# Kernel optimization log

Hardware: AMD Instinct MI355X
Metric: run time of the kernel (lower is better)

The kernel has to match this reference:

```python
import jax, jax.numpy as jnp
import numpy as np

C = 512        # feat_dim
T_LEN = 8192   # sequence length
N = 16384      # number of proposals
HID = 1024     # hidden_dim
OUT = 512      # out_dim
RATIO = 0.15   # boundary_ratio


def setup_inputs() -> dict:
    key = jax.random.key(0)
    ks = jax.random.split(key, 6)
    feat_map = jax.random.normal(ks[0], (C, T_LEN), jnp.float32)
    l = jax.random.randint(ks[1], (N,), 0, T_LEN - 64)
    width = jax.random.randint(ks[2], (N,), 8, 512)
    r = jnp.minimum(l + width, T_LEN - 1)
    W1 = jax.random.normal(ks[3], (HID, 2 * C), jnp.float32) * 0.02
    b1 = jnp.zeros((HID,), jnp.float32)
    W2 = jax.random.normal(ks[4], (OUT, HID), jnp.float32) * 0.02
    b2 = jnp.zeros((OUT,), jnp.float32)
    return {
        "feat_map": feat_map,
        "l": l.astype(jnp.int32),
        "r": r.astype(jnp.int32),
        "T": T_LEN,
        "W1": W1, "b1": b1, "W2": W2, "b2": b2,
    }


def _boundary_regions(l, r, T):
    # Mirrors: w = max(r-l, 1.0); bw = max(1, int(ratio*w)); clipped windows.
    lf = l.astype(jnp.float32)
    rf = r.astype(jnp.float32)
    w = jnp.maximum(rf - lf, 1.0)
    bw = jnp.maximum(1, (RATIO * w).astype(jnp.int32))  # int() truncation (w > 0)
    rl = jnp.round(lf).astype(jnp.int32)
    rr = jnp.round(rf).astype(jnp.int32)
    lb_s = jnp.maximum(0, rl - bw)
    lb_e = jnp.minimum(T, rl + bw)
    rb_s = jnp.maximum(0, rr - bw)
    rb_e = jnp.minimum(T, rr + bw)
    return lb_s, lb_e, rb_s, rb_e


def _pool(cs, s, e, T):
    # mean of feat[:, s:e] via inclusive prefix sums; cs: (C, T+1)
    e = jnp.maximum(s + 1, e)
    e = jnp.minimum(e, T)
    seg = cs[:, e] - cs[:, s]                      # (C, N)
    return (seg / (e - s).astype(cs.dtype)).T      # (N, C)


def reference(feat_map, l, r, T, W1, b1, W2, b2):
    # feat_map: (C, T); l, r: (N,) int proposal boundaries
    cs = jnp.concatenate(
        [jnp.zeros((feat_map.shape[0], 1), feat_map.dtype),
         jnp.cumsum(feat_map, axis=1)], axis=1)    # (C, T+1)
    lb_s, lb_e, rb_s, rb_e = _boundary_regions(l, r, T)
    e_left = _pool(cs, lb_s, lb_e, T)              # (N, C)
    e_right = _pool(cs, rb_s, rb_e, T)             # (N, C)
    e = jnp.concatenate([e_left, e_right], axis=-1)  # (N, 2C)
    h = jax.nn.relu(e @ W1.T + b1)                 # (N, HID)
    return h @ W2.T + b2                           # (N, OUT)
```

## Files before the change

kernel.cpp:

```cpp
#include <hip/hip_runtime.h>
#include <hip/hip_bf16.h>
#include <stdint.h>

#define C_DIM 512
#define T_SEQ 8192
#define N_PROP 16384
#define HID_DIM 1024
#define OUT_DIM 512
#define K2C 1024

typedef __attribute__((ext_vector_type(8))) __bf16 bf16x8;
typedef __attribute__((ext_vector_type(4))) float f32x4;

__global__ __launch_bounds__(256) void cumsum_kernel(const float* __restrict__ feat,
                                                     float* __restrict__ cs_inc) {
    int c = blockIdx.x;
    const float4* in = (const float4*)(feat + (size_t)c * T_SEQ);
    float4* out = (float4*)(cs_inc + (size_t)c * T_SEQ);
    const int lane = threadIdx.x & 63;
    const int w = threadIdx.x >> 6;
    __shared__ float wsum[4];

    float4 v[8];
    float carry = 0.0f;
#pragma unroll
    for (int i = 0; i < 8; ++i) {
        float4 t = in[w * 512 + i * 64 + lane];
        float a1 = t.x + t.y;
        float a2 = a1 + t.z;
        float a3 = a2 + t.w;
        float x = a3;
#pragma unroll
        for (int s = 1; s < 64; s <<= 1) {
            float y = __shfl_up(x, s);
            if (lane >= s) x += y;
        }
        float base = carry + (x - a3);
        v[i].x = base + t.x;
        v[i].y = base + a1;
        v[i].z = base + a2;
        v[i].w = base + a3;
        carry += __shfl(x, 63);
    }
    if (lane == 0) wsum[w] = carry;
    __syncthreads();
    float pre = 0.0f;
    for (int j = 0; j < 4; ++j)
        if (j < w) pre += wsum[j];
#pragma unroll
    for (int i = 0; i < 8; ++i) {
        float4 o;
        o.x = v[i].x + pre; o.y = v[i].y + pre; o.z = v[i].z + pre; o.w = v[i].w + pre;
        out[w * 512 + i * 64 + lane] = o;
    }
}

__global__ __launch_bounds__(256) void transpose_kernel(const float* __restrict__ cs_inc,
                                                        float* __restrict__ cs_t) {
    __shared__ float tl[32][33];
    int tx = threadIdx.x, ty = threadIdx.y;
    int x0 = blockIdx.x * 32;
    int y0 = blockIdx.y * 32;
#pragma unroll
    for (int i = 0; i < 32; i += 8) {
        int t = x0 + tx;
        int ch = y0 + ty + i;
        float v = 0.0f;
        if (t >= 1 && t <= T_SEQ) v = cs_inc[(size_t)ch * T_SEQ + (t - 1)];
        tl[ty + i][tx] = v;
    }
    __syncthreads();
#pragma unroll
    for (int i = 0; i < 32; i += 8) {
        int t = x0 + ty + i;
        int ch = y0 + tx;
        if (t <= T_SEQ) cs_t[(size_t)t * C_DIM + ch] = tl[tx][ty + i];
    }
}

__global__ __launch_bounds__(512) void pool_kernel(const float* __restrict__ cs_t,
                                                   const int* __restrict__ lptr,
                                                   const int* __restrict__ rptr,
                                                   __hip_bfloat16* __restrict__ e) {
    int n = blockIdx.x * 4 + (threadIdx.x >> 7);
    int c4 = (threadIdx.x & 127) * 4;
    int li = lptr[n], ri = rptr[n];
    float w = fmaxf((float)(ri - li), 1.0f);
    int bw = max(1, (int)(0.15f * w));
    int lb_s = max(0, li - bw);
    int lb_e = min(T_SEQ, li + bw);
    int rb_s = max(0, ri - bw);
    int rb_e = min(T_SEQ, ri + bw);
    lb_e = min(max(lb_s + 1, lb_e), T_SEQ);
    rb_e = min(max(rb_s + 1, rb_e), T_SEQ);
    float4 a = *(const float4*)(cs_t + (size_t)lb_e * C_DIM + c4);
    float4 b = *(const float4*)(cs_t + (size_t)lb_s * C_DIM + c4);
    float4 cc = *(const float4*)(cs_t + (size_t)rb_e * C_DIM + c4);
    float4 d = *(const float4*)(cs_t + (size_t)rb_s * C_DIM + c4);
    float rl = 1.0f / (float)(lb_e - lb_s);
    float rr = 1.0f / (float)(rb_e - rb_s);
    __hip_bfloat16 L0 = __float2bfloat16((a.x - b.x) * rl);
    __hip_bfloat16 L1 = __float2bfloat16((a.y - b.y) * rl);
    __hip_bfloat16 L2 = __float2bfloat16((a.z - b.z) * rl);
    __hip_bfloat16 L3 = __float2bfloat16((a.w - b.w) * rl);
    __hip_bfloat16 R0 = __float2bfloat16((cc.x - d.x) * rr);
    __hip_bfloat16 R1 = __float2bfloat16((cc.y - d.y) * rr);
    __hip_bfloat16 R2 = __float2bfloat16((cc.z - d.z) * rr);
    __hip_bfloat16 R3 = __float2bfloat16((cc.w - d.w) * rr);
    ushort4 ul, ur;
    ul.x = *(unsigned short*)&L0; ul.y = *(unsigned short*)&L1;
    ul.z = *(unsigned short*)&L2; ul.w = *(unsigned short*)&L3;
    ur.x = *(unsigned short*)&R0; ur.y = *(unsigned short*)&R1;
    ur.z = *(unsigned short*)&R2; ur.w = *(unsigned short*)&R3;
    *(ushort4*)(e + (size_t)n * K2C + c4) = ul;
    *(ushort4*)(e + (size_t)n * K2C + C_DIM + c4) = ur;
}

__global__ __launch_bounds__(256) void cvt_bf16_kernel(const float* __restrict__ W1,
                                                       const float* __restrict__ W2,
                                                       __hip_bfloat16* __restrict__ W1b,
                                                       __hip_bfloat16* __restrict__ W2b) {
    const int n1 = HID_DIM * K2C;
    int i = (blockIdx.x * 256 + threadIdx.x) * 4;
    const float* src;
    __hip_bfloat16* dst;
    int j;
    if (i < n1) { src = W1; dst = W1b; j = i; }
    else        { src = W2; dst = W2b; j = i - n1; }
    float4 v = *(const float4*)(src + j);
    __hip_bfloat16 h0 = __float2bfloat16(v.x);
    __hip_bfloat16 h1 = __float2bfloat16(v.y);
    __hip_bfloat16 h2 = __float2bfloat16(v.z);
    __hip_bfloat16 h3 = __float2bfloat16(v.w);
    ushort4 u;
    u.x = *(unsigned short*)&h0; u.y = *(unsigned short*)&h1;
    u.z = *(unsigned short*)&h2; u.w = *(unsigned short*)&h3;
    *(ushort4*)(dst + j) = u;
}

template <int BM, int BN, int WM, int WN, int K, int RELU_BF16>
__global__ __launch_bounds__(512, 2) void gemm_hi_kernel(const __hip_bfloat16* __restrict__ A,
                                                         const __hip_bfloat16* __restrict__ B,
                                                         const float* __restrict__ bias,
                                                         void* __restrict__ Cout,
                                                         int Nc, int NBlk) {
    constexpr int BK = 32;
    constexpr int NT = K / BK;
    constexpr int WMT = BM / WM, WNT = BN / WN;
    constexpr int MR = WMT / 16, NR = WNT / 16;
    constexpr int RA = BM / 128;
    constexpr int RB = BN / 128;
    constexpr bool BHALF = (BN % 128) == 64;

    __shared__ __align__(16) __hip_bfloat16 As[2][BM * BK];
    __shared__ __align__(16) __hip_bfloat16 Bs[2][BN * BK];

    const int tid = threadIdx.x;
    const int lane = tid & 63;
    const int wid = tid >> 6;
    const int wm = wid / WN;
    const int wn = wid % WN;

    const int nwg = gridDim.x;
    const int wg = (blockIdx.x & 7) * (nwg >> 3) + (blockIdx.x >> 3);
    const long m0 = (long)(wg / NBlk) * BM;
    const long n0 = (long)(wg % NBlk) * BN;

    const int phase = ((blockIdx.x >> 8) & 1) * (NT / 2);

    const int srow = tid >> 2;
    const int sgsw = (tid & 3) ^ (srow & 3);
    const int fr = lane & 15;
    const int gq = lane >> 4;

    f32x4 acc[MR][NR] = {};

    auto stage = [&](int s, int k0) {
#pragma unroll
        for (int i = 0; i < RA; ++i)
            __builtin_amdgcn_global_load_lds(
                (const __attribute__((address_space(1))) void*)(A + (m0 + i * 128 + srow) * K + k0 + sgsw * 8),
                (__attribute__((address_space(3))) void*)(&As[s][i * 4096 + tid * 8]), 16, 0, 0);
#pragma unroll
        for (int i = 0; i < RB; ++i)
            __builtin_amdgcn_global_load_lds(
                (const __attribute__((address_space(1))) void*)(B + (n0 + i * 128 + srow) * K + k0 + sgsw * 8),
                (__attribute__((address_space(3))) void*)(&Bs[s][i * 4096 + tid * 8]), 16, 0, 0);
        if constexpr (BHALF) {
            if (tid < 256)
                __builtin_amdgcn_global_load_lds(
                    (const __attribute__((address_space(1))) void*)(B + (n0 + srow) * K + k0 + sgsw * 8),
                    (__attribute__((address_space(3))) void*)(&Bs[s][tid * 8]), 16, 0, 0);
        }
    };
    auto ldA = [&](int s, int row) -> bf16x8 {
        return *(const bf16x8*)(&As[s][row * BK + ((gq ^ (row & 3)) * 8)]);
    };
    auto ldB = [&](int s, int row) -> bf16x8 {
        return *(const bf16x8*)(&Bs[s][row * BK + ((gq ^ (row & 3)) * 8)]);
    };

    stage(0, phase * BK);
    __syncthreads();
    for (int t = 0; t < NT; ++t) {
        const int cur = t & 1;
        if (t + 1 < NT) stage(cur ^ 1, (((t + 1 + phase) & (NT - 1)) * BK));
        bf16x8 af[MR], bv[NR];
#pragma unroll
        for (int m = 0; m < MR; ++m) af[m] = ldA(cur, wm * WMT + m * 16 + fr);
#pragma unroll
        for (int n = 0; n < NR; ++n) bv[n] = ldB(cur, wn * WNT + n * 16 + fr);
#pragma unroll
        for (int m = 0; m < MR; ++m)
#pragma unroll
            for (int n = 0; n < NR; ++n)
                acc[m][n] = __builtin_amdgcn_mfma_f32_16x16x32_bf16(af[m], bv[n], acc[m][n], 0, 0, 0);
        __syncthreads();
    }

    const int rq = (lane >> 4) * 4;
#pragma unroll
    for (int m = 0; m < MR; ++m)
#pragma unroll
        for (int n = 0; n < NR; ++n) {
            long col = n0 + wn * WNT + n * 16 + fr;
            float bb = bias[col];
#pragma unroll
            for (int q = 0; q < 4; ++q) {
                long row = m0 + wm * WMT + m * 16 + rq + q;
                float v = acc[m][n][q] + bb;
                if (RELU_BF16) {
                    v = fmaxf(v, 0.0f);
                    ((__hip_bfloat16*)Cout)[row * Nc + col] = __float2bfloat16(v);
                } else {
                    ((float*)Cout)[row * Nc + col] = v;
                }
            }
        }
}

extern "C" void kernel_launch(void* const* d_in, const int* in_sizes, int n_in,
                              void* d_out, int out_size, void* d_ws, size_t ws_size,
                              hipStream_t stream) {
    const float* feat = (const float*)d_in[0];
    const int* l = (const int*)d_in[1];
    const int* r = (const int*)d_in[2];
    const float* W1 = (const float*)d_in[4];
    const float* b1 = (const float*)d_in[5];
    const float* W2 = (const float*)d_in[6];
    const float* b2 = (const float*)d_in[7];

    char* ws = (char*)d_ws;
    float* cs_t = (float*)ws;
    __hip_bfloat16* e = (__hip_bfloat16*)(ws + 16779264);
    __hip_bfloat16* h = (__hip_bfloat16*)(ws + 50333696);
    float* cs_inc = (float*)(ws + 50333696);
    __hip_bfloat16* W1b = (__hip_bfloat16*)(ws + 83888128);
    __hip_bfloat16* W2b = (__hip_bfloat16*)(ws + 85985280);

    const int ncvt = (HID_DIM * K2C + OUT_DIM * HID_DIM) / 4 / 256;
    cvt_bf16_kernel<<<dim3(ncvt), 256, 0, stream>>>(W1, W2, W1b, W2b);
    cumsum_kernel<<<dim3(C_DIM), 256, 0, stream>>>(feat, cs_inc);
    transpose_kernel<<<dim3((T_SEQ + 32) / 32, C_DIM / 32), dim3(32, 8), 0, stream>>>(cs_inc, cs_t);
    pool_kernel<<<dim3(N_PROP / 4), 512, 0, stream>>>(cs_t, l, r, e);

    gemm_hi_kernel<256, 128, 4, 2, K2C, 1>
        <<<dim3((N_PROP / 256) * (HID_DIM / 128)), 512, 0, stream>>>(e, W1b, b1, h, HID_DIM, HID_DIM / 128);
    gemm_hi_kernel<256, 64, 8, 1, HID_DIM, 0>
        <<<dim3((N_PROP / 256) * (OUT_DIM / 64)), 512, 0, stream>>>(h, W2b, b2, d_out, OUT_DIM, OUT_DIM / 64);
}
```

Before: 117.7 us.

## Rewrite GEMM kernels with BK=64, larger tiles and fine-grained staged pipeline

Replaces the simple double-buffered GEMM with a hand-scheduled kernel that uses BK=64, a 256x256 or 256x128 tile per workgroup, and interleaves half-tile async global-to-LDS loads with MFMA groups separated by explicit barriers, waitcnts and setprio. The goal is to overlap memory staging with matrix-core work and raise arithmetic intensity per LDS load. In exchange, occupancy drops to one workgroup per CU, the grid gets smaller, and the many barriers add synchronization overhead.

```diff
diff --git a/kernel.cpp b/kernel.cpp
--- a/kernel.cpp
+++ b/kernel.cpp
@@ -11,6 +11,9 @@
 
 typedef __attribute__((ext_vector_type(8))) __bf16 bf16x8;
 typedef __attribute__((ext_vector_type(4))) float f32x4;
+
+#define BAR() __builtin_amdgcn_s_barrier()
+#define LGKM0_SB() do { asm volatile("s_waitcnt lgkmcnt(0)" ::: "memory"); __builtin_amdgcn_sched_barrier(0); } while (0)
 
 __global__ __launch_bounds__(256) void cumsum_kernel(const float* __restrict__ feat,
                                                      float* __restrict__ cs_inc) {
@@ -138,19 +141,18 @@
     *(ushort4*)(dst + j) = u;
 }
 
-template <int BM, int BN, int WM, int WN, int K, int RELU_BF16>
-__global__ __launch_bounds__(512, 2) void gemm_hi_kernel(const __hip_bfloat16* __restrict__ A,
+template <int BN, int K, int RELU_BF16>
+__global__ __launch_bounds__(512, 1) void gemm_hk_kernel(const __hip_bfloat16* __restrict__ A,
                                                          const __hip_bfloat16* __restrict__ B,
                                                          const float* __restrict__ bias,
                                                          void* __restrict__ Cout,
                                                          int Nc, int NBlk) {
-    constexpr int BK = 32;
-    constexpr int NT = K / BK;
-    constexpr int WMT = BM / WM, WNT = BN / WN;
-    constexpr int MR = WMT / 16, NR = WNT / 16;
-    constexpr int RA = BM / 128;
-    constexpr int RB = BN / 128;
-    constexpr bool BHALF = (BN % 128) == 64;
+    constexpr int BM = 256, BK = 64;
+    constexpr int NT = K / BK, NI = NT / 2;
+    constexpr int WNT = BN / 4;
+    constexpr int NR = WNT / 16;
+    constexpr int RBH = BN / 128;
+    constexpr int BHR = BN / 2;
 
     __shared__ __align__(16) __hip_bfloat16 As[2][BM * BK];
     __shared__ __align__(16) __hip_bfloat16 Bs[2][BN * BK];
@@ -158,76 +160,126 @@
     const int tid = threadIdx.x;
     const int lane = tid & 63;
     const int wid = tid >> 6;
-    const int wm = wid / WN;
-    const int wn = wid % WN;
+    const int wm = wid >> 2;
+    const int wn = wid & 3;
 
     const int nwg = gridDim.x;
     const int wg = (blockIdx.x & 7) * (nwg >> 3) + (blockIdx.x >> 3);
     const long m0 = (long)(wg / NBlk) * BM;
     const long n0 = (long)(wg % NBlk) * BN;
 
-    const int phase = ((blockIdx.x >> 8) & 1) * (NT / 2);
-
-    const int srow = tid >> 2;
-    const int sgsw = (tid & 3) ^ (srow & 3);
+    const int srow = tid >> 3;
+    const int schunk = (tid & 7) ^ (srow & 7);
     const int fr = lane & 15;
-    const int gq = lane >> 4;
-
-    f32x4 acc[MR][NR] = {};
-
-    auto stage = [&](int s, int k0) {
-#pragma unroll
-        for (int i = 0; i < RA; ++i)
+    const int g8 = (lane >> 4) * 8;
+
+    f32x4 acc[8][NR] = {};
+
+    auto stA = [&](int d, int h, long kel) {
+#pragma unroll
+        for (int r2 = 0; r2 < 2; ++r2)
             __builtin_amdgcn_global_load_lds(
-                (const __attribute__((address_space(1))) void*)(A + (m0 + i * 128 + srow) * K + k0 + sgsw * 8),
-                (__attribute__((address_space(3))) void*)(&As[s][i * 4096 + tid * 8]), 16, 0, 0);
-#pragma unroll
-        for (int i = 0; i < RB; ++i)
+                (const __attribute__((address_space(1))) void*)(A + (m0 + h * 128 + r2 * 64 + srow) * K + kel + schunk * 8),
+                (__attribute__((address_space(3))) void*)(&As[d][(h * 128 + r2 * 64) * 64 + tid * 8]), 16, 0, 0);
+    };
+    auto stB = [&](int d, int h, long kel) {
+#pragma unroll
+        for (int r2 = 0; r2 < RBH; ++r2)
             __builtin_amdgcn_global_load_lds(
-                (const __attribute__((address_space(1))) void*)(B + (n0 + i * 128 + srow) * K + k0 + sgsw * 8),
-                (__attribute__((address_space(3))) void*)(&Bs[s][i * 4096 + tid * 8]), 16, 0, 0);
-        if constexpr (BHALF) {
-            if (tid < 256)
-                __builtin_amdgcn_global_load_lds(
-                    (const __attribute__((address_space(1))) void*)(B + (n0 + srow) * K + k0 + sgsw * 8),
-                    (__attribute__((address_space(3))) void*)(&Bs[s][tid * 8]), 16, 0, 0);
-        }
-    };
-    auto ldA = [&](int s, int row) -> bf16x8 {
-        return *(const bf16x8*)(&As[s][row * BK + ((gq ^ (row & 3)) * 8)]);
-    };
-    auto ldB = [&](int s, int row) -> bf16x8 {
-        return *(const bf16x8*)(&Bs[s][row * BK + ((gq ^ (row & 3)) * 8)]);
-    };
-
-    stage(0, phase * BK);
-    __syncthreads();
-    for (int t = 0; t < NT; ++t) {
-        const int cur = t & 1;
-        if (t + 1 < NT) stage(cur ^ 1, (((t + 1 + phase) & (NT - 1)) * BK));
-        bf16x8 af[MR], bv[NR];
-#pragma unroll
-        for (int m = 0; m < MR; ++m) af[m] = ldA(cur, wm * WMT + m * 16 + fr);
-#pragma unroll
-        for (int n = 0; n < NR; ++n) bv[n] = ldB(cur, wn * WNT + n * 16 + fr);
-#pragma unroll
-        for (int m = 0; m < MR; ++m)
+                (const __attribute__((address_space(1))) void*)(B + (n0 + h * BHR + r2 * 64 + srow) * K + kel + schunk * 8),
+                (__attribute__((address_space(3))) void*)(&Bs[d][(h * BHR + r2 * 64) * 64 + tid * 8]), 16, 0, 0);
+    };
+    auto ldf = [&](const __hip_bfloat16* buf, int row, int kb) -> bf16x8 {
+        return *(const bf16x8*)(&buf[row * 64 + ((kb + g8) ^ ((row & 7) * 8))]);
+    };
+    auto rdA = [&](int d, int mlo, int kb, bf16x8* af) {
+#pragma unroll
+        for (int m = 0; m < 4; ++m) af[m] = ldf(&As[d][0], wm * 128 + (mlo + m) * 16 + fr, kb);
+    };
+    auto rdB = [&](int d, int kb, bf16x8* bv) {
+#pragma unroll
+        for (int n = 0; n < NR; ++n) bv[n] = ldf(&Bs[d][0], wn * WNT + n * 16 + fr, kb);
+    };
+    auto mf4 = [&](const bf16x8* af, const bf16x8* bv, int mlo) {
+        __builtin_amdgcn_s_setprio(1);
+#pragma unroll
+        for (int m = 0; m < 4; ++m)
 #pragma unroll
             for (int n = 0; n < NR; ++n)
-                acc[m][n] = __builtin_amdgcn_mfma_f32_16x16x32_bf16(af[m], bv[n], acc[m][n], 0, 0, 0);
-        __syncthreads();
+                acc[mlo + m][n] = __builtin_amdgcn_mfma_f32_16x16x32_bf16(af[m], bv[n], acc[mlo + m][n], 0, 0, 0);
+        __builtin_amdgcn_s_setprio(0);
+    };
+
+    stA(0, 0, 0); stA(0, 1, 0); stB(0, 0, 0); stB(0, 1, 0);
+    stB(1, 0, BK);
+    asm volatile("s_waitcnt vmcnt(%0)" ::"n"(RBH) : "memory");
+    BAR();
+
+    bf16x8 afA[4], afB[4], bv[NR];
+
+#pragma unroll 1
+    for (int i = 0; i < NI; ++i) {
+        const bool more = (i + 1 < NI);
+        const long kU1 = (2L * i + 1) * BK;
+        const long kE = (2L * i + 2) * BK;
+        const long kO = (2L * i + 3) * BK;
+
+        rdA(0, 0, 0, afA); rdB(0, 0, bv);
+        stB(1, 1, kU1);
+        BAR(); LGKM0_SB();
+        mf4(afA, bv, 0);
+        BAR();
+        rdA(0, 4, 0, afB);
+        stA(1, 0, kU1);
+        BAR(); LGKM0_SB();
+        mf4(afB, bv, 4);
+        BAR();
+        rdA(0, 0, 32, afA); rdB(0, 32, bv);
+        stA(1, 1, kU1);
+        BAR(); LGKM0_SB();
+        mf4(afA, bv, 0);
+        BAR();
+        rdA(0, 4, 32, afB);
+        if (more) stB(0, 0, kE);
+        BAR(); LGKM0_SB();
+        mf4(afB, bv, 4);
+        if (more) asm volatile("s_waitcnt vmcnt(%0)" ::"n"(RBH) : "memory");
+        else      asm volatile("s_waitcnt vmcnt(0)" ::: "memory");
+        BAR();
+        rdA(1, 0, 0, afA); rdB(1, 0, bv);
+        if (more) stB(0, 1, kE);
+        BAR(); LGKM0_SB();
+        mf4(afA, bv, 0);
+        BAR();
+        rdA(1, 4, 0, afB);
+        if (more) stA(0, 0, kE);
+        BAR(); LGKM0_SB();
+        mf4(afB, bv, 4);
+        BAR();
+        rdA(1, 0, 32, afA); rdB(1, 32, bv);
+        if (more) stA(0, 1, kE);
+        BAR(); LGKM0_SB();
+        mf4(afA, bv, 0);
+        BAR();
+        rdA(1, 4, 32, afB);
+        if (more) stB(1, 0, kO);
+        BAR(); LGKM0_SB();
+        mf4(afB, bv, 4);
+        if (more) asm volatile("s_waitcnt vmcnt(%0)" ::"n"(RBH) : "memory");
+        else      asm volatile("s_waitcnt vmcnt(0)" ::: "memory");
+        BAR();
     }
 
     const int rq = (lane >> 4) * 4;
 #pragma unroll
-    for (int m = 0; m < MR; ++m)
+    for (int m = 0; m < 8; ++m)
 #pragma unroll
         for (int n = 0; n < NR; ++n) {
             long col = n0 + wn * WNT + n * 16 + fr;
             float bb = bias[col];
 #pragma unroll
             for (int q = 0; q < 4; ++q) {
-                long row = m0 + wm * WMT + m * 16 + rq + q;
+                long row = m0 + wm * 128 + m * 16 + rq + q;
                 float v = acc[m][n][q] + bb;
                 if (RELU_BF16) {
                     v = fmaxf(v, 0.0f);
@@ -264,8 +316,8 @@
     transpose_kernel<<<dim3((T_SEQ + 32) / 32, C_DIM / 32), dim3(32, 8), 0, stream>>>(cs_inc, cs_t);
     pool_kernel<<<dim3(N_PROP / 4), 512, 0, stream>>>(cs_t, l, r, e);
 
-    gemm_hi_kernel<256, 128, 4, 2, K2C, 1>
-        <<<dim3((N_PROP / 256) * (HID_DIM / 128)), 512, 0, stream>>>(e, W1b, b1, h, HID_DIM, HID_DIM / 128);
-    gemm_hi_kernel<256, 64, 8, 1, HID_DIM, 0>
-        <<<dim3((N_PROP / 256) * (OUT_DIM / 64)), 512, 0, stream>>>(h, W2b, b2, d_out, OUT_DIM, OUT_DIM / 64);
-}
+    gemm_hk_kernel<256, K2C, 1>
+        <<<dim3((N_PROP / 256) * (HID_DIM / 256)), 512, 0, stream>>>(e, W1b, b1, h, HID_DIM, HID_DIM / 256);
+    gemm_hk_kernel<128, HID_DIM, 0>
+        <<<dim3((N_PROP / 256) * (OUT_DIM / 128)), 512, 0, stream>>>(h, W2b, b2, d_out, OUT_DIM, OUT_DIM / 128);
+}
```

After: 113.7 us. -3.4%, faster.

## Retile GEMMs to 256-wide tiles with BK=64 and fuse prep kernels

Applied to the files above, without the earlier changes.

Replaces the 512-thread GEMM with a 256-thread, 2x2-wave kernel using larger output tiles (256x256 and 256x128), BK=64 with an 8-way XOR LDS swizzle, and removes the K-phase staggering. It also merges the weight bf16 conversion and the cumsum into a single launch. The intent is higher data reuse per LDS byte and one fewer launch. The cost is heavy register and LDS pressure, with only one workgroup per CU.

```diff
diff --git a/kernel.cpp b/kernel.cpp
--- a/kernel.cpp
+++ b/kernel.cpp
@@ -12,46 +12,65 @@
 typedef __attribute__((ext_vector_type(8))) __bf16 bf16x8;
 typedef __attribute__((ext_vector_type(4))) float f32x4;
 
-__global__ __launch_bounds__(256) void cumsum_kernel(const float* __restrict__ feat,
-                                                     float* __restrict__ cs_inc) {
-    int c = blockIdx.x;
-    const float4* in = (const float4*)(feat + (size_t)c * T_SEQ);
-    float4* out = (float4*)(cs_inc + (size_t)c * T_SEQ);
-    const int lane = threadIdx.x & 63;
-    const int w = threadIdx.x >> 6;
-    __shared__ float wsum[4];
-
-    float4 v[8];
-    float carry = 0.0f;
-#pragma unroll
-    for (int i = 0; i < 8; ++i) {
-        float4 t = in[w * 512 + i * 64 + lane];
-        float a1 = t.x + t.y;
-        float a2 = a1 + t.z;
-        float a3 = a2 + t.w;
-        float x = a3;
-#pragma unroll
-        for (int s = 1; s < 64; s <<= 1) {
-            float y = __shfl_up(x, s);
-            if (lane >= s) x += y;
-        }
-        float base = carry + (x - a3);
-        v[i].x = base + t.x;
-        v[i].y = base + a1;
-        v[i].z = base + a2;
-        v[i].w = base + a3;
-        carry += __shfl(x, 63);
-    }
-    if (lane == 0) wsum[w] = carry;
-    __syncthreads();
-    float pre = 0.0f;
-    for (int j = 0; j < 4; ++j)
-        if (j < w) pre += wsum[j];
-#pragma unroll
-    for (int i = 0; i < 8; ++i) {
-        float4 o;
-        o.x = v[i].x + pre; o.y = v[i].y + pre; o.z = v[i].z + pre; o.w = v[i].w + pre;
-        out[w * 512 + i * 64 + lane] = o;
+__global__ __launch_bounds__(256) void pre_kernel(const float* __restrict__ feat,
+                                                  float* __restrict__ cs_inc,
+                                                  const float* __restrict__ W1,
+                                                  const float* __restrict__ W2,
+                                                  __hip_bfloat16* __restrict__ W1b,
+                                                  __hip_bfloat16* __restrict__ W2b) {
+    if (blockIdx.x < C_DIM) {
+        int c = blockIdx.x;
+        const float4* in = (const float4*)(feat + (size_t)c * T_SEQ);
+        float4* out = (float4*)(cs_inc + (size_t)c * T_SEQ);
+        const int lane = threadIdx.x & 63;
+        const int w = threadIdx.x >> 6;
+        __shared__ float wsum[4];
+        float4 v[8];
+        float carry = 0.0f;
+#pragma unroll
+        for (int i = 0; i < 8; ++i) {
+            float4 t = in[w * 512 + i * 64 + lane];
+            float a1 = t.x + t.y;
+            float a2 = a1 + t.z;
+            float a3 = a2 + t.w;
+            float x = a3;
+#pragma unroll
+            for (int s = 1; s < 64; s <<= 1) {
+                float y = __shfl_up(x, s);
+                if (lane >= s) x += y;
+            }
+            float base = carry + (x - a3);
+            v[i].x = base + t.x; v[i].y = base + a1; v[i].z = base + a2; v[i].w = base + a3;
+            carry += __shfl(x, 63);
+        }
+        if (lane == 0) wsum[w] = carry;
+        __syncthreads();
+        float pre = 0.0f;
+        for (int j = 0; j < 4; ++j)
+            if (j < w) pre += wsum[j];
+#pragma unroll
+        for (int i = 0; i < 8; ++i) {
+            float4 o;
+            o.x = v[i].x + pre; o.y = v[i].y + pre; o.z = v[i].z + pre; o.w = v[i].w + pre;
+            out[w * 512 + i * 64 + lane] = o;
+        }
+    } else {
+        const int n1 = HID_DIM * K2C;
+        int i = ((blockIdx.x - C_DIM) * 256 + threadIdx.x) * 4;
+        const float* src;
+        __hip_bfloat16* dst;
+        int j;
+        if (i < n1) { src = W1; dst = W1b; j = i; }
+        else        { src = W2; dst = W2b; j = i - n1; }
+        float4 v = *(const float4*)(src + j);
+        __hip_bfloat16 h0 = __float2bfloat16(v.x);
+        __hip_bfloat16 h1 = __float2bfloat16(v.y);
+        __hip_bfloat16 h2 = __float2bfloat16(v.z);
+        __hip_bfloat16 h3 = __float2bfloat16(v.w);
+        ushort4 u;
+        u.x = *(unsigned short*)&h0; u.y = *(unsigned short*)&h1;
+        u.z = *(unsigned short*)&h2; u.w = *(unsigned short*)&h3;
+        *(ushort4*)(dst + j) = u;
     }
 }
 
@@ -116,41 +135,17 @@
     *(ushort4*)(e + (size_t)n * K2C + C_DIM + c4) = ur;
 }
 
-__global__ __launch_bounds__(256) void cvt_bf16_kernel(const float* __restrict__ W1,
-                                                       const float* __restrict__ W2,
-                                                       __hip_bfloat16* __restrict__ W1b,
-                                                       __hip_bfloat16* __restrict__ W2b) {
-    const int n1 = HID_DIM * K2C;
-    int i = (blockIdx.x * 256 + threadIdx.x) * 4;
-    const float* src;
-    __hip_bfloat16* dst;
-    int j;
-    if (i < n1) { src = W1; dst = W1b; j = i; }
-    else        { src = W2; dst = W2b; j = i - n1; }
-    float4 v = *(const float4*)(src + j);
-    __hip_bfloat16 h0 = __float2bfloat16(v.x);
-    __hip_bfloat16 h1 = __float2bfloat16(v.y);
-    __hip_bfloat16 h2 = __float2bfloat16(v.z);
-    __hip_bfloat16 h3 = __float2bfloat16(v.w);
-    ushort4 u;
-    u.x = *(unsigned short*)&h0; u.y = *(unsigned short*)&h1;
-    u.z = *(unsigned short*)&h2; u.w = *(unsigned short*)&h3;
-    *(ushort4*)(dst + j) = u;
-}
-
-template <int BM, int BN, int WM, int WN, int K, int RELU_BF16>
-__global__ __launch_bounds__(512, 2) void gemm_hi_kernel(const __hip_bfloat16* __restrict__ A,
+template <int BM, int BN, int K, int RELU_BF16>
+__global__ __launch_bounds__(256, 1) void gemm_bw_kernel(const __hip_bfloat16* __restrict__ A,
                                                          const __hip_bfloat16* __restrict__ B,
                                                          const float* __restrict__ bias,
                                                          void* __restrict__ Cout,
                                                          int Nc, int NBlk) {
-    constexpr int BK = 32;
+    constexpr int BK = 64;
     constexpr int NT = K / BK;
-    constexpr int WMT = BM / WM, WNT = BN / WN;
+    constexpr int WMT = BM / 2, WNT = BN / 2;
     constexpr int MR = WMT / 16, NR = WNT / 16;
-    constexpr int RA = BM / 128;
-    constexpr int RB = BN / 128;
-    constexpr bool BHALF = (BN % 128) == 64;
+    constexpr int RA = BM / 32, RB = BN / 32;
 
     __shared__ __align__(16) __hip_bfloat16 As[2][BM * BK];
     __shared__ __align__(16) __hip_bfloat16 Bs[2][BN * BK];
@@ -158,63 +153,57 @@
     const int tid = threadIdx.x;
     const int lane = tid & 63;
     const int wid = tid >> 6;
-    const int wm = wid / WN;
-    const int wn = wid % WN;
+    const int wm = wid >> 1, wn = wid & 1;
 
     const int nwg = gridDim.x;
     const int wg = (blockIdx.x & 7) * (nwg >> 3) + (blockIdx.x >> 3);
     const long m0 = (long)(wg / NBlk) * BM;
     const long n0 = (long)(wg % NBlk) * BN;
 
-    const int phase = ((blockIdx.x >> 8) & 1) * (NT / 2);
-
-    const int srow = tid >> 2;
-    const int sgsw = (tid & 3) ^ (srow & 3);
+    const int srow = tid >> 3;
+    const int schunk = (tid & 7) ^ (srow & 7);
     const int fr = lane & 15;
-    const int gq = lane >> 4;
+    const int g8 = (lane >> 4) * 8;
 
     f32x4 acc[MR][NR] = {};
 
-    auto stage = [&](int s, int k0) {
+    auto stage = [&](int s, long k0) {
 #pragma unroll
         for (int i = 0; i < RA; ++i)
             __builtin_amdgcn_global_load_lds(
-                (const __attribute__((address_space(1))) void*)(A + (m0 + i * 128 + srow) * K + k0 + sgsw * 8),
-                (__attribute__((address_space(3))) void*)(&As[s][i * 4096 + tid * 8]), 16, 0, 0);
+                (const __attribute__((address_space(1))) void*)(A + (m0 + i * 32 + srow) * K + k0 + schunk * 8),
+                (__attribute__((address_space(3))) void*)(&As[s][i * 2048 + tid * 8]), 16, 0, 0);
 #pragma unroll
         for (int i = 0; i < RB; ++i)
             __builtin_amdgcn_global_load_lds(
-                (const __attribute__((address_space(1))) void*)(B + (n0 + i * 128 + srow) * K + k0 + sgsw * 8),
-                (__attribute__((address_space(3))) void*)(&Bs[s][i * 4096 + tid * 8]), 16, 0, 0);
-        if constexpr (BHALF) {
-            if (tid < 256)
-                __builtin_amdgcn_global_load_lds(
-                    (const __attribute__((address_space(1))) void*)(B + (n0 + srow) * K + k0 + sgsw * 8),
-                    (__attribute__((address_space(3))) void*)(&Bs[s][tid * 8]), 16, 0, 0);
-        }
+                (const __attribute__((address_space(1))) void*)(B + (n0 + i * 32 + srow) * K + k0 + schunk * 8),
+                (__attribute__((address_space(3))) void*)(&Bs[s][i * 2048 + tid * 8]), 16, 0, 0);
     };
-    auto ldA = [&](int s, int row) -> bf16x8 {
-        return *(const bf16x8*)(&As[s][row * BK + ((gq ^ (row & 3)) * 8)]);
+    auto ldA = [&](int s, int row, int kb) -> bf16x8 {
+        return *(const bf16x8*)(&As[s][row * BK + ((kb + g8) ^ ((row & 7) * 8))]);
     };
-    auto ldB = [&](int s, int row) -> bf16x8 {
-        return *(const bf16x8*)(&Bs[s][row * BK + ((gq ^ (row & 3)) * 8)]);
+    auto ldB = [&](int s, int row, int kb) -> bf16x8 {
+        return *(const bf16x8*)(&Bs[s][row * BK + ((kb + g8) ^ ((row & 7) * 8))]);
     };
 
-    stage(0, phase * BK);
+    stage(0, 0);
     __syncthreads();
     for (int t = 0; t < NT; ++t) {
         const int cur = t & 1;
-        if (t + 1 < NT) stage(cur ^ 1, (((t + 1 + phase) & (NT - 1)) * BK));
-        bf16x8 af[MR], bv[NR];
-#pragma unroll
-        for (int m = 0; m < MR; ++m) af[m] = ldA(cur, wm * WMT + m * 16 + fr);
-#pragma unroll
-        for (int n = 0; n < NR; ++n) bv[n] = ldB(cur, wn * WNT + n * 16 + fr);
-#pragma unroll
-        for (int m = 0; m < MR; ++m)
-#pragma unroll
-            for (int n = 0; n < NR; ++n)
-                acc[m][n] = __builtin_amdgcn_mfma_f32_16x16x32_bf16(af[m], bv[n], acc[m][n], 0, 0, 0);
+        if (t + 1 < NT) stage(cur ^ 1, (long)(t + 1) * BK);
+#pragma unroll
+        for (int kk = 0; kk < 2; ++kk) {
+            bf16x8 af[MR], bv[NR];
+#pragma unroll
+            for (int m = 0; m < MR; ++m) af[m] = ldA(cur, wm * WMT + m * 16 + fr, kk * 32);
+#pragma unroll
+            for (int n = 0; n < NR; ++n) bv[n] = ldB(cur, wn * WNT + n * 16 + fr, kk * 32);
+#pragma unroll
+            for (int m = 0; m < MR; ++m)
+#pragma unroll
+                for (int n = 0; n < NR; ++n)
+                    acc[m][n] = __builtin_amdgcn_mfma_f32_16x16x32_bf16(af[m], bv[n], acc[m][n], 0, 0, 0);
+        }
         __syncthreads();
     }
 
@@ -259,13 +248,12 @@
     __hip_bfloat16* W2b = (__hip_bfloat16*)(ws + 85985280);
 
     const int ncvt = (HID_DIM * K2C + OUT_DIM * HID_DIM) / 4 / 256;
-    cvt_bf16_kernel<<<dim3(ncvt), 256, 0, stream>>>(W1, W2, W1b, W2b);
-    cumsum_kernel<<<dim3(C_DIM), 256, 0, stream>>>(feat, cs_inc);
+    pre_kernel<<<dim3(C_DIM + ncvt), 256, 0, stream>>>(feat, cs_inc, W1, W2, W1b, W2b);
     transpose_kernel<<<dim3((T_SEQ + 32) / 32, C_DIM / 32), dim3(32, 8), 0, stream>>>(cs_inc, cs_t);
     pool_kernel<<<dim3(N_PROP / 4), 512, 0, stream>>>(cs_t, l, r, e);
 
-    gemm_hi_kernel<256, 128, 4, 2, K2C, 1>
-        <<<dim3((N_PROP / 256) * (HID_DIM / 128)), 512, 0, stream>>>(e, W1b, b1, h, HID_DIM, HID_DIM / 128);
-    gemm_hi_kernel<256, 64, 8, 1, HID_DIM, 0>
-        <<<dim3((N_PROP / 256) * (OUT_DIM / 64)), 512, 0, stream>>>(h, W2b, b2, d_out, OUT_DIM, OUT_DIM / 64);
-}
+    gemm_bw_kernel<256, 256, K2C, 1>
+        <<<dim3((N_PROP / 256) * (HID_DIM / 256)), 256, 0, stream>>>(e, W1b, b1, h, HID_DIM, HID_DIM / 256);
+    gemm_bw_kernel<256, 128, HID_DIM, 0>
+        <<<dim3((N_PROP / 256) * (OUT_DIM / 128)), 256, 0, stream>>>(h, W2b, b2, d_out, OUT_DIM, OUT_DIM / 128);
+}
```

Result: slower. 139.1 us (+18.2%).
